# Optimization experiments

Measured on AMD Instinct MI355X. Metric: run time of the kernel, lower is better.

The kernel has to match this reference:

```python
import jax, jax.numpy as jnp
import numpy as np

DIM = 1024
NUM_HEADS = 16
D_HEAD = DIM // NUM_HEADS  # 64
N_SEQ = 1605               # 1600 patch tokens + 5 prefix (cls+registers)
HW = 1600


def setup_inputs() -> dict:
    key = jax.random.key(0)
    kx, kr, kq, kp, kb = jax.random.split(key, 5)
    x = jax.random.normal(kx, (N_SEQ, DIM), dtype=jnp.float32)
    # rope = stack([sin, cos]) of per-position, per-channel angles
    angles = jax.random.uniform(kr, (HW, D_HEAD), dtype=jnp.float32) * (2.0 * np.pi)
    rope = jnp.stack([jnp.sin(angles), jnp.cos(angles)], axis=0)  # [2, hw, d_head]
    W_qkv = jax.random.normal(kq, (3 * DIM, DIM), dtype=jnp.float32)
    W_proj = jax.random.normal(kp, (DIM, DIM), dtype=jnp.float32)
    b_proj = jax.random.normal(kb, (DIM,), dtype=jnp.float32)
    return {"x": x, "rope": rope, "W_qkv": W_qkv, "W_proj": W_proj, "b_proj": b_proj}


def _rope_apply(t, sin, cos):
    # t: [hw, n_head, d_head]; sin/cos: [hw, d_head]
    half = t.shape[-1] // 2
    rot = jnp.concatenate([-t[..., half:], t[..., :half]], axis=-1)  # rotate_half
    return t * cos[:, None, :] + rot * sin[:, None, :]


def reference(x, rope, W_qkv, W_proj, b_proj):
    n_seq = x.shape[0]
    qkv = x @ W_qkv.T                                   # [n_seq, 3*dim]
    qkv = qkv.reshape(n_seq, 3, NUM_HEADS, D_HEAD)
    q, k, v = qkv[:, 0], qkv[:, 1], qkv[:, 2]           # [n_seq, nh, dh]
    sin, cos = rope[0], rope[1]
    prefix = n_seq - sin.shape[0]
    q = jnp.concatenate([q[:prefix], _rope_apply(q[prefix:], sin, cos)], axis=0)
    k = jnp.concatenate([k[:prefix], _rope_apply(k[prefix:], sin, cos)], axis=0)
    scale = 1.0 / np.sqrt(D_HEAD)
    scores = jnp.einsum("qhd,khd->hqk", q, k) * scale   # [nh, n_seq, n_seq]
    attn = jax.nn.softmax(scores, axis=-1)
    out = jnp.einsum("hqk,khd->qhd", attn, v)           # [n_seq, nh, dh]
    out = out.reshape(n_seq, DIM)
    return out @ W_proj.T + b_proj
```

## Files before the change

### kernel.cpp

```cpp
#include <hip/hip_runtime.h>
#include <hip/hip_bf16.h>

#define DIM    1024
#define NH     16
#define DH     64
#define NSEQ   1605
#define HWIN   1600
#define PREFIX 5
#define NSEQP  1664
#define KX     3072

typedef __bf16 bf16_t;
typedef bf16_t bf16x4 __attribute__((ext_vector_type(4)));
typedef bf16_t bf16x8 __attribute__((ext_vector_type(8)));
typedef float  f32x4  __attribute__((ext_vector_type(4)));
typedef unsigned short u16;

#define MFMA(a,b,c) __builtin_amdgcn_mfma_f32_16x16x32_bf16(a,b,c,0,0,0)

union BU { bf16_t b; u16 u; };

template<int ROWS>
__device__ __forceinline__ void stage64(const bf16_t* __restrict__ seg,
                                        int row0, int ldk, int kin,
                                        bf16_t* lds, int tid)
{
    const int l = tid & 63, w = tid >> 6;
#pragma unroll
    for (int i = 0; i < ROWS / 32; ++i) {
        const int rb = i * 32 + w * 8;
        const int r  = rb + (l >> 3);
        const int p  = l & 7;
        const bf16_t* src = seg + (size_t)(row0 + r) * ldk + kin + ((p ^ (r & 7)) << 3);
        __builtin_amdgcn_global_load_lds(
            (const __attribute__((address_space(1))) void*)src,
            (__attribute__((address_space(3))) void*)(lds + rb * 64),
            16, 0, 0);
    }
}

__device__ __forceinline__ bf16x8 frag(const bf16_t* lds, int row, int ch) {
    return *(const bf16x8*)&lds[row * 64 + ((ch ^ (row & 7)) << 3)];
}

#define NX4 (NSEQP * 256)
#define NQ4 (3072 * 256)
#define NP4 (1024 * 256)

__global__ __launch_bounds__(256) void prep_kernel(
    const float* __restrict__ x, const float* __restrict__ Wq,
    const float* __restrict__ Wp,
    bf16_t* __restrict__ xh, bf16_t* __restrict__ xl,
    bf16_t* __restrict__ wqh, bf16_t* __restrict__ wql,
    bf16_t* __restrict__ wph, bf16_t* __restrict__ wpl)
{
    const int i = blockIdx.x * 256 + threadIdx.x;
    if (i >= NX4 + NQ4 + NP4) return;
    float4 v = make_float4(0.f, 0.f, 0.f, 0.f);
    bf16_t *ph, *pl;
    size_t off;
    if (i < NX4) {
        if ((i >> 8) < NSEQ) v = ((const float4*)x)[i];
        ph = xh; pl = xl; off = (size_t)i * 4;
    } else if (i < NX4 + NQ4) {
        int j = i - NX4;
        v = ((const float4*)Wq)[j];
        ph = wqh; pl = wql; off = (size_t)j * 4;
    } else {
        int j = i - NX4 - NQ4;
        v = ((const float4*)Wp)[j];
        ph = wph; pl = wpl; off = (size_t)j * 4;
    }
    bf16_t h0 = (bf16_t)v.x, h1 = (bf16_t)v.y, h2 = (bf16_t)v.z, h3 = (bf16_t)v.w;
    bf16x4 hv = {h0, h1, h2, h3};
    bf16x4 lv = {(bf16_t)(v.x - (float)h0), (bf16_t)(v.y - (float)h1),
                 (bf16_t)(v.z - (float)h2), (bf16_t)(v.w - (float)h3)};
    *(bf16x4*)(ph + off) = hv;
    *(bf16x4*)(pl + off) = lv;
}

__global__ __launch_bounds__(256, 2) void gemm_qkv(
    const bf16_t* __restrict__ xh, const bf16_t* __restrict__ xl,
    const bf16_t* __restrict__ wqh, const bf16_t* __restrict__ wql,
    const float* __restrict__ rope,
    bf16_t* __restrict__ Qhi, bf16_t* __restrict__ Qlo,
    bf16_t* __restrict__ Khi, bf16_t* __restrict__ Klo,
    bf16_t* __restrict__ Vt)
{
    __shared__ bf16_t As[2][64 * 64];
    __shared__ bf16_t Bs[2][128 * 64];

    const int lin = blockIdx.y * 24 + blockIdx.x;
    const int xcd = lin & 7, idx = lin >> 3;
    const int m0 = (idx / 3) * 64;
    const int n0 = (xcd * 3 + idx % 3) * 128;

    const int tid = threadIdx.x;
    const int w = tid >> 6, l = tid & 63, lr = l & 15, lg = l >> 4;
    const int wr = (w >> 1) * 32, wc = (w & 1) * 64;

    f32x4 acc[2][4] = {};

    auto stage = [&](int buf, int kt) {
        const int k0 = kt * 64, sg = k0 >> 10, kin = k0 & 1023;
        const bf16_t* Aseg = (sg == 1) ? xl : xh;
        const bf16_t* Bseg = (sg == 2) ? wql : wqh;
        stage64<64>(Aseg, m0, 1024, kin, As[buf], tid);
        stage64<128>(Bseg, n0, 1024, kin, Bs[buf], tid);
    };

    stage(0, 0);
    __syncthreads();
    int cur = 0;
    for (int kt = 0; kt < KX / 64; ++kt) {
        if (kt + 1 < KX / 64) stage(cur ^ 1, kt + 1);
#pragma unroll
        for (int ks = 0; ks < 2; ++ks) {
            bf16x8 a[2];
#pragma unroll
            for (int rt = 0; rt < 2; ++rt) a[rt] = frag(As[cur], wr + 16 * rt + lr, ks * 4 + lg);
#pragma unroll
            for (int ct = 0; ct < 4; ++ct) {
                bf16x8 b = frag(Bs[cur], wc + 16 * ct + lr, ks * 4 + lg);
#pragma unroll
                for (int rt = 0; rt < 2; ++rt)
                    acc[rt][ct] = MFMA(a[rt], b, acc[rt][ct]);
            }
        }
        __syncthreads();
        cur ^= 1;
    }

    const int which = n0 >> 10;
    const int cbase = (n0 & 1023) + wc;
    const float qscale = (which == 0) ? 0.125f : 1.0f;
    const float* sinp = rope;
    const float* cosp = rope + (size_t)HWIN * DH;

#pragma unroll
    for (int ct = 0; ct < 4; ++ct) {
        const int col = cbase + 16 * ct + lr;
        const int hd = col >> 6, dd = col & 63;
#pragma unroll
        for (int rt = 0; rt < 2; ++rt) {
            const int sbase = m0 + wr + 16 * rt + 4 * lg;
            if (sbase >= NSEQ) continue;
            if (which == 2) {
                size_t off = ((size_t)hd * DH + dd) * NSEQP + sbase;
                if (sbase + 3 < NSEQ) {
                    BU t0, t1, t2, t3;
                    t0.b = (bf16_t)acc[rt][ct][0]; t1.b = (bf16_t)acc[rt][ct][1];
                    t2.b = (bf16_t)acc[rt][ct][2]; t3.b = (bf16_t)acc[rt][ct][3];
                    *(ushort4*)((u16*)Vt + off) = make_ushort4(t0.u, t1.u, t2.u, t3.u);
                } else {
#pragma unroll
                    for (int reg = 0; reg < 4; ++reg)
                        if (sbase + reg < NSEQ)
                            Vt[off + reg] = (bf16_t)acc[rt][ct][reg];
                }
            } else {
#pragma unroll
                for (int reg = 0; reg < 4; ++reg) {
                    const int seq = sbase + reg;
                    if (seq >= NSEQ) continue;
                    float val = acc[rt][ct][reg] * qscale;
                    float o = val;
                    if (seq >= PREFIX) {
                        float partner = acc[rt][ct ^ 2][reg] * qscale;
                        float rot = (dd < 32) ? -partner : partner;
                        float sn = sinp[(size_t)(seq - PREFIX) * DH + dd];
                        float cs = cosp[(size_t)(seq - PREFIX) * DH + dd];
                        o = val * cs + rot * sn;
                    }
                    bf16_t hh = (bf16_t)o;
                    bf16_t ll = (bf16_t)(o - (float)hh);
                    size_t off = ((size_t)hd * NSEQP + seq) * DH + dd;
                    if (which == 0) { Qhi[off] = hh; Qlo[off] = ll; }
                    else            { Khi[off] = hh; Klo[off] = ll; }
                }
            }
        }
    }
}

#define ASTRH 72
#define NJT   (NSEQP / 64)

__global__ __launch_bounds__(256, 2) void attn_kernel(
    const bf16_t* __restrict__ Qhi, const bf16_t* __restrict__ Qlo,
    const bf16_t* __restrict__ Khi, const bf16_t* __restrict__ Klo,
    const bf16_t* __restrict__ Vt,
    bf16_t* __restrict__ Oh, bf16_t* __restrict__ Ol)
{
    __shared__ bf16_t Ksh[2][64 * 64], Ksl[2][64 * 64], Vsh[2][64 * 64];
    __shared__ bf16_t PS[4][16 * ASTRH];

    const int lin = blockIdx.y * 26 + blockIdx.x;
    const int xcd = lin & 7, idx = lin >> 3;
    const int h = 2 * xcd + idx / 26;
    const int q0 = (idx % 26) * 64;

    const int tid = threadIdx.x, w = tid >> 6, l = tid & 63;
    const int lr = l & 15, lg = l >> 4;

    bf16x8 qh[2], ql[2];
    {
        const size_t qoff = ((size_t)h * NSEQP + q0 + 16 * w + lr) * DH;
#pragma unroll
        for (int ks = 0; ks < 2; ++ks) {
            qh[ks] = *(const bf16x8*)&Qhi[qoff + 32 * ks + 8 * lg];
            ql[ks] = *(const bf16x8*)&Qlo[qoff + 32 * ks + 8 * lg];
        }
    }

    const bf16_t* KbH = Khi + (size_t)h * NSEQP * DH;
    const bf16_t* KbL = Klo + (size_t)h * NSEQP * DH;
    const bf16_t* Vb  = Vt  + (size_t)h * DH * NSEQP;

    f32x4 o[4] = {};
    float m[4], lsum[4];
#pragma unroll
    for (int r = 0; r < 4; ++r) { m[r] = -1e30f; lsum[r] = 0.f; }

    auto stage_kv = [&](int buf, int jt) {
        const int j0 = jt * 64;
        stage64<64>(KbH, j0, 64, 0, Ksh[buf], tid);
        stage64<64>(KbL, j0, 64, 0, Ksl[buf], tid);
        stage64<64>(Vb, 0, NSEQP, j0, Vsh[buf], tid);
    };

    stage_kv(0, 0);
    __syncthreads();
    int cur = 0;
    for (int jt = 0; jt < NJT; ++jt) {
        const int j0 = jt * 64;
        if (jt + 1 < NJT) stage_kv(cur ^ 1, jt + 1);

        f32x4 s[4] = {};
        __builtin_amdgcn_s_setprio(1);
#pragma unroll
        for (int ct = 0; ct < 4; ++ct) {
#pragma unroll
            for (int ks = 0; ks < 2; ++ks) {
                bf16x8 bh = frag(Ksh[cur], 16 * ct + lr, ks * 4 + lg);
                bf16x8 bl = frag(Ksl[cur], 16 * ct + lr, ks * 4 + lg);
                s[ct] = MFMA(ql[ks], bh, s[ct]);
                s[ct] = MFMA(qh[ks], bl, s[ct]);
                s[ct] = MFMA(qh[ks], bh, s[ct]);
            }
        }
        __builtin_amdgcn_s_setprio(0);
#pragma unroll
        for (int ct = 0; ct < 4; ++ct) {
            if (j0 + 16 * ct + lr >= NSEQ) {
                s[ct][0] = -1e30f; s[ct][1] = -1e30f;
                s[ct][2] = -1e30f; s[ct][3] = -1e30f;
            }
        }

        float so[4];
#pragma unroll
        for (int reg = 0; reg < 4; ++reg) {
            float mt = fmaxf(fmaxf(s[0][reg], s[1][reg]), fmaxf(s[2][reg], s[3][reg]));
#pragma unroll
            for (int off = 1; off < 16; off <<= 1)
                mt = fmaxf(mt, __shfl_xor(mt, off));
            float mn = fmaxf(m[reg], mt);
            so[reg] = __expf(m[reg] - mn);
            m[reg] = mn;
            float psum = 0.f;
#pragma unroll
            for (int ct = 0; ct < 4; ++ct) {
                float pv = __expf(s[ct][reg] - mn);
                s[ct][reg] = pv;
                psum += pv;
            }
#pragma unroll
            for (int off = 1; off < 16; off <<= 1)
                psum += __shfl_xor(psum, off);
            lsum[reg] = lsum[reg] * so[reg] + psum;
        }

#pragma unroll
        for (int ct = 0; ct < 4; ++ct)
#pragma unroll
            for (int reg = 0; reg < 4; ++reg)
                PS[w][(4 * lg + reg) * ASTRH + 16 * ct + lr] = (bf16_t)s[ct][reg];

#pragma unroll
        for (int ctd = 0; ctd < 4; ++ctd)
#pragma unroll
            for (int reg = 0; reg < 4; ++reg)
                o[ctd][reg] *= so[reg];

        __builtin_amdgcn_s_setprio(1);
#pragma unroll
        for (int ks = 0; ks < 2; ++ks) {
            bf16x8 pa = *(const bf16x8*)&PS[w][lr * ASTRH + 32 * ks + 8 * lg];
#pragma unroll
            for (int ctd = 0; ctd < 4; ++ctd) {
                bf16x8 vb = frag(Vsh[cur], 16 * ctd + lr, ks * 4 + lg);
                o[ctd] = MFMA(pa, vb, o[ctd]);
            }
        }
        __builtin_amdgcn_s_setprio(0);

        __syncthreads();
        cur ^= 1;
    }

#pragma unroll
    for (int ctd = 0; ctd < 4; ++ctd) {
#pragma unroll
        for (int reg = 0; reg < 4; ++reg) {
            const int seq = q0 + 16 * w + 4 * lg + reg;
            if (seq < NSEQ) {
                float ov = o[ctd][reg] / lsum[reg];
                bf16_t hi = (bf16_t)ov;
                bf16_t lo = (bf16_t)(ov - (float)hi);
                size_t oo = (size_t)seq * DIM + h * DH + 16 * ctd + lr;
                Oh[oo] = hi; Ol[oo] = lo;
            }
        }
    }
}

__global__ __launch_bounds__(256, 2) void gemm_proj(
    const bf16_t* __restrict__ oh, const bf16_t* __restrict__ ol,
    const bf16_t* __restrict__ wph, const bf16_t* __restrict__ wpl,
    const float* __restrict__ bias, float* __restrict__ C)
{
    __shared__ bf16_t As[2][64 * 64];
    __shared__ bf16_t Bs[2][64 * 64];

    const int lin = blockIdx.y * 16 + blockIdx.x;
    const int xcd = lin & 7, idx = lin >> 3;
    const int m0 = (idx >> 1) * 64;
    const int n0 = ((xcd << 1) | (idx & 1)) * 64;

    const int tid = threadIdx.x;
    const int w = tid >> 6, l = tid & 63, lr = l & 15, lg = l >> 4;
    const int wr = (w >> 1) * 32, wc = (w & 1) * 32;

    f32x4 acc[2][2] = {};

    auto stage = [&](int buf, int kt) {
        const int k0 = kt * 64, sg = k0 >> 10, kin = k0 & 1023;
        const bf16_t* Aseg = (sg == 1) ? ol : oh;
        const bf16_t* Bseg = (sg == 2) ? wpl : wph;
        stage64<64>(Aseg, m0, 1024, kin, As[buf], tid);
        stage64<64>(Bseg, n0, 1024, kin, Bs[buf], tid);
    };

    stage(0, 0);
    __syncthreads();
    int cur = 0;
    for (int kt = 0; kt < KX / 64; ++kt) {
        if (kt + 1 < KX / 64) stage(cur ^ 1, kt + 1);
#pragma unroll
        for (int ks = 0; ks < 2; ++ks) {
            bf16x8 a[2];
#pragma unroll
            for (int rt = 0; rt < 2; ++rt) a[rt] = frag(As[cur], wr + 16 * rt + lr, ks * 4 + lg);
#pragma unroll
            for (int ct = 0; ct < 2; ++ct) {
                bf16x8 b = frag(Bs[cur], wc + 16 * ct + lr, ks * 4 + lg);
#pragma unroll
                for (int rt = 0; rt < 2; ++rt)
                    acc[rt][ct] = MFMA(a[rt], b, acc[rt][ct]);
            }
        }
        __syncthreads();
        cur ^= 1;
    }

#pragma unroll
    for (int ct = 0; ct < 2; ++ct) {
        const int n = n0 + wc + 16 * ct + lr;
        const float bv = bias[n];
#pragma unroll
        for (int rt = 0; rt < 2; ++rt) {
#pragma unroll
            for (int reg = 0; reg < 4; ++reg) {
                const int seq = m0 + wr + 16 * rt + 4 * lg + reg;
                if (seq < NSEQ)
                    C[(size_t)seq * DIM + n] = acc[rt][ct][reg] + bv;
            }
        }
    }
}

extern "C" void kernel_launch(void* const* d_in, const int* in_sizes, int n_in,
                              void* d_out, int out_size, void* d_ws, size_t ws_size,
                              hipStream_t stream)
{
    const float* x     = (const float*)d_in[0];
    const float* rope  = (const float*)d_in[1];
    const float* Wqkv  = (const float*)d_in[2];
    const float* Wproj = (const float*)d_in[3];
    const float* bproj = (const float*)d_in[4];
    float* out = (float*)d_out;

    const size_t XE  = (size_t)NSEQP * 1024;
    const size_t WQE = (size_t)3072 * 1024;
    const size_t WPE = (size_t)1024 * 1024;
    const size_t HSE = (size_t)NH * NSEQP * DH;

    bf16_t* p = (bf16_t*)d_ws;
    bf16_t* xh  = p; p += XE;
    bf16_t* xl  = p; p += XE;
    bf16_t* wqh = p; p += WQE;
    bf16_t* wql = p; p += WQE;
    bf16_t* wph = p; p += WPE;
    bf16_t* wpl = p; p += WPE;
    bf16_t* Qhi = p; p += HSE;
    bf16_t* Qlo = p; p += HSE;
    bf16_t* Khi = p; p += HSE;
    bf16_t* Klo = p; p += HSE;
    bf16_t* Vt  = p; p += HSE;
    bf16_t* Oh  = xh;
    bf16_t* Ol  = xl;

    const int PTOT = NX4 + NQ4 + NP4;
    prep_kernel<<<(PTOT + 255) / 256, 256, 0, stream>>>(
        x, Wqkv, Wproj, xh, xl, wqh, wql, wph, wpl);

    gemm_qkv<<<dim3(24, NSEQP / 64), 256, 0, stream>>>(
        xh, xl, wqh, wql, rope, Qhi, Qlo, Khi, Klo, Vt);

    attn_kernel<<<dim3(26, NH), 256, 0, stream>>>(
        Qhi, Qlo, Khi, Klo, Vt, Oh, Ol);

    gemm_proj<<<dim3(16, NSEQP / 64), 256, 0, stream>>>(
        Oh, Ol, wph, wpl, bproj, out);
}
```

Before: 224.6 us.

## Split attention KV range across two blocks and merge partials

The attention kernel now launches a third grid dimension that splits the 26 key tiles into two halves. Each half writes an unnormalized bf16 partial output plus its running max and sum. A new merge kernel combines the two halves with log-sum-exp rescaling and emits the hi/lo bf16 outputs. This doubles the block count from 416 to 832 to fill more CUs, and masking now runs only on the last tile. In exchange it adds partial-output traffic, one extra launch, and precision loss from storing partials as single bf16 instead of a hi/lo pair.

```diff
diff --git a/kernel.cpp b/kernel.cpp
--- a/kernel.cpp
+++ b/kernel.cpp
@@ -185,12 +185,13 @@
 
 #define ASTRH 72
 #define NJT   (NSEQP / 64)
+#define TPS   (NJT / 2)
 
 __global__ __launch_bounds__(256, 2) void attn_kernel(
     const bf16_t* __restrict__ Qhi, const bf16_t* __restrict__ Qlo,
     const bf16_t* __restrict__ Khi, const bf16_t* __restrict__ Klo,
     const bf16_t* __restrict__ Vt,
-    bf16_t* __restrict__ Oh, bf16_t* __restrict__ Ol)
+    bf16_t* __restrict__ Opart, float* __restrict__ Oml)
 {
     __shared__ bf16_t Ksh[2][64 * 64], Ksl[2][64 * 64], Vsh[2][64 * 64];
     __shared__ bf16_t PS[4][16 * ASTRH];
@@ -199,6 +200,8 @@
     const int xcd = lin & 7, idx = lin >> 3;
     const int h = 2 * xcd + idx / 26;
     const int q0 = (idx % 26) * 64;
+    const int split = blockIdx.z;
+    const int jt0 = split * TPS, jtend = jt0 + TPS;
 
     const int tid = threadIdx.x, w = tid >> 6, l = tid & 63;
     const int lr = l & 15, lg = l >> 4;
@@ -229,12 +232,12 @@
         stage64<64>(Vb, 0, NSEQP, j0, Vsh[buf], tid);
     };
 
-    stage_kv(0, 0);
+    stage_kv(0, jt0);
     __syncthreads();
     int cur = 0;
-    for (int jt = 0; jt < NJT; ++jt) {
+    for (int jt = jt0; jt < jtend; ++jt) {
         const int j0 = jt * 64;
-        if (jt + 1 < NJT) stage_kv(cur ^ 1, jt + 1);
+        if (jt + 1 < jtend) stage_kv(cur ^ 1, jt + 1);
 
         f32x4 s[4] = {};
         __builtin_amdgcn_s_setprio(1);
@@ -250,11 +253,14 @@
             }
         }
         __builtin_amdgcn_s_setprio(0);
-#pragma unroll
-        for (int ct = 0; ct < 4; ++ct) {
-            if (j0 + 16 * ct + lr >= NSEQ) {
-                s[ct][0] = -1e30f; s[ct][1] = -1e30f;
-                s[ct][2] = -1e30f; s[ct][3] = -1e30f;
+
+        if (jt == NJT - 1) {
+#pragma unroll
+            for (int ct = 0; ct < 4; ++ct) {
+                if (j0 + 16 * ct + lr >= NSEQ) {
+                    s[ct][0] = -1e30f; s[ct][1] = -1e30f;
+                    s[ct][2] = -1e30f; s[ct][3] = -1e30f;
+                }
             }
         }
 
@@ -309,20 +315,58 @@
         cur ^= 1;
     }
 
+    const size_t sb = ((size_t)split * NH + h) * NSEQP;
 #pragma unroll
     for (int ctd = 0; ctd < 4; ++ctd) {
+#pragma unroll
+        for (int reg = 0; reg < 4; ++reg) {
+            const int seq = q0 + 16 * w + 4 * lg + reg;
+            if (seq < NSEQ)
+                Opart[(sb + seq) * DH + 16 * ctd + lr] = (bf16_t)o[ctd][reg];
+        }
+    }
+    if (lr == 0) {
 #pragma unroll
         for (int reg = 0; reg < 4; ++reg) {
             const int seq = q0 + 16 * w + 4 * lg + reg;
             if (seq < NSEQ) {
-                float ov = o[ctd][reg] / lsum[reg];
-                bf16_t hi = (bf16_t)ov;
-                bf16_t lo = (bf16_t)(ov - (float)hi);
-                size_t oo = (size_t)seq * DIM + h * DH + 16 * ctd + lr;
-                Oh[oo] = hi; Ol[oo] = lo;
-            }
-        }
-    }
+                Oml[(sb + seq) * 2 + 0] = m[reg];
+                Oml[(sb + seq) * 2 + 1] = lsum[reg];
+            }
+        }
+    }
+}
+
+__global__ __launch_bounds__(256) void merge_kernel(
+    const bf16_t* __restrict__ Opart, const float* __restrict__ Oml,
+    bf16_t* __restrict__ Oh, bf16_t* __restrict__ Ol)
+{
+    const int h = blockIdx.y;
+    const int q = blockIdx.x * 16 + (threadIdx.x >> 4);
+    const int d4 = (threadIdx.x & 15) * 4;
+    if (q >= NSEQ) return;
+
+    const size_t i0 = (size_t)h * NSEQP + q;
+    const size_t i1 = ((size_t)NH + h) * NSEQP + q;
+    const float m0 = Oml[i0 * 2], l0 = Oml[i0 * 2 + 1];
+    const float m1 = Oml[i1 * 2], l1 = Oml[i1 * 2 + 1];
+    const float M = fmaxf(m0, m1);
+    const float a0 = __expf(m0 - M), a1 = __expf(m1 - M);
+    const float inv = 1.0f / (l0 * a0 + l1 * a1);
+
+    bf16x4 o0 = *(const bf16x4*)&Opart[i0 * DH + d4];
+    bf16x4 o1 = *(const bf16x4*)&Opart[i1 * DH + d4];
+    bf16x4 hv, lv;
+#pragma unroll
+    for (int j = 0; j < 4; ++j) {
+        float v = (a0 * (float)o0[j] + a1 * (float)o1[j]) * inv;
+        bf16_t hi = (bf16_t)v;
+        hv[j] = hi;
+        lv[j] = (bf16_t)(v - (float)hi);
+    }
+    const size_t oo = (size_t)q * DIM + h * DH + d4;
+    *(bf16x4*)&Oh[oo] = hv;
+    *(bf16x4*)&Ol[oo] = lv;
 }
 
 __global__ __launch_bounds__(256, 2) void gemm_proj(
@@ -418,6 +462,8 @@
     bf16_t* Khi = p; p += HSE;
     bf16_t* Klo = p; p += HSE;
     bf16_t* Vt  = p; p += HSE;
+    bf16_t* Opart = p; p += 2 * HSE;
+    float*  Oml   = (float*)p;
     bf16_t* Oh  = xh;
     bf16_t* Ol  = xl;
 
@@ -428,8 +474,11 @@
     gemm_qkv<<<dim3(24, NSEQP / 64), 256, 0, stream>>>(
         xh, xl, wqh, wql, rope, Qhi, Qlo, Khi, Klo, Vt);
 
-    attn_kernel<<<dim3(26, NH), 256, 0, stream>>>(
-        Qhi, Qlo, Khi, Klo, Vt, Oh, Ol);
+    attn_kernel<<<dim3(26, NH, 2), 256, 0, stream>>>(
+        Qhi, Qlo, Khi, Klo, Vt, Opart, Oml);
+
+    merge_kernel<<<dim3(NSEQP / 16, NH), 256, 0, stream>>>(
+        Opart, Oml, Oh, Ol);
 
     gemm_proj<<<dim3(16, NSEQP / 64), 256, 0, stream>>>(
         Oh, Ol, wph, wpl, bproj, out);
```

Result: no change. 228.9 us (+1.9%).
